# Kernel optimization log

Hardware: AMD Instinct MI355X
Metric: run time of the kernel (lower is better)

The kernel has to match this reference:

```python
import math
import jax, jax.numpy as jnp
import numpy as np

ANCHORS_SETTINGS = (
    dict(layer='p3', stride=32, size=48, scale=[2 ** (1.0 / 3.0), 2 ** (2.0 / 3.0)], aspect_ratio=[0.667, 1, 1.5]),
    dict(layer='p4', stride=64, size=96, scale=[2 ** (1.0 / 3.0), 2 ** (2.0 / 3.0)], aspect_ratio=[0.667, 1, 1.5]),
    dict(layer='p5', stride=128, size=192, scale=[1, 2 ** (1.0 / 3.0), 2 ** (2.0 / 3.0)], aspect_ratio=[0.667, 1, 1.5]),
)


def anchor_configs():
    # 21 static (kernel, stride, padding) configs, in the exact counter order of
    # weighted_anchor_aggregator (p3 x6, p4 x6, p5 x9).
    cfgs = []
    for info in ANCHORS_SETTINGS:
        stride, size = info['stride'], info['size']
        for scale in info['scale']:
            for ar in info['aspect_ratio']:
                kernel = (int(size * scale / float(ar) ** 0.5), int(size * scale * float(ar) ** 0.5))
                padding = (math.ceil((kernel[0] - stride) / 2.0), math.ceil((kernel[1] - stride) / 2.0))
                cfgs.append((kernel, (stride, stride), padding))
    return cfgs


def extract_weighted_patches(x, weights, kernel, stride, padding):
    # x: (B,H,W,C); weights: (B,k,gh,gw). Vectorized equivalent of the original
    # lax.scan over per-position dynamic_slice gathers:
    #   acc = sum_{i,j} weights[:,:,i,j] (x) x_pad[:, i*s : i*s+kh, j*s : j*s+kw, :]
    b = x.shape[0]
    _, k, gh, gw = weights.shape
    xp = jnp.pad(x, ((0, 0),
                     (padding[0], padding[0] + kernel[0]),
                     (padding[1], padding[1] + kernel[1]),
                     (0, 0)))
    rows = jnp.arange(gh)[:, None] * stride[0] + jnp.arange(kernel[0])[None, :]  # (gh, kh)
    cols = jnp.arange(gw)[:, None] * stride[1] + jnp.arange(kernel[1])[None, :]  # (gw, kw)
    # gather all strided patches: (B, gh, kh, gw, kw, C)
    patches = xp[:, rows][:, :, :, cols]
    # weighted sum over grid positions -> (B, k, kh, kw, C)
    return jnp.einsum('bkij,bihjwc->bkhwc', weights, patches)


def _aggregate(x, weights_p3, weights_p4, weights_p5):
    weights = ([weights_p3[:, a] for a in range(weights_p3.shape[1])]
               + [weights_p4[:, a] for a in range(weights_p4.shape[1])]
               + [weights_p5[:, a] for a in range(weights_p5.shape[1])])
    b, k = weights[0].shape[0], weights[0].shape[1]
    acc = jnp.zeros((b * k, 224, 224, 3), x.dtype)
    for w, (kernel, stride, padding) in zip(weights, anchor_configs()):
        agg = extract_weighted_patches(x, w, kernel, stride, padding)
        agg = agg.reshape(b * k, kernel[0], kernel[1], 3)
        acc = acc + jax.image.resize(agg, (b * k, 224, 224, 3), 'bilinear')
    return acc


def setup_inputs() -> dict:
    key = jax.random.key(0)
    k0, k1, k2, k3 = jax.random.split(key, 4)
    B, K = 8, 4
    return {
        'x': jax.random.normal(k0, (B, 448, 448, 3), jnp.float32),
        'weights_p3': jax.random.uniform(k1, (B, 6, K, 14, 14), jnp.float32),
        'weights_p4': jax.random.uniform(k2, (B, 6, K, 7, 7), jnp.float32),
        'weights_p5': jax.random.uniform(k3, (B, 9, K, 4, 4), jnp.float32),
    }


def reference(x, weights_p3, weights_p4, weights_p5):
    return _aggregate(x, weights_p3, weights_p4, weights_p5)
```

## Files before the change

### kernel.cpp

```cpp
#include <hip/hip_runtime.h>
#include <math.h>


#define BATCH 8
#define KK 4
#define OUT_HW 224
#define IMG_HW 448
#define NCFG 21

#define WTBL_BYTES (NCFG * 2 * OUT_HW * 16)
#define ITBL_BYTES (NCFG * 2 * OUT_HW * 4)
#define WT_OFF_BYTES (WTBL_BYTES + ITBL_BYTES)
#define WT_F4 12912
#define AGG_OFF_BYTES (WT_OFF_BYTES + WT_F4 * 16)

#define REGION_PX 640

struct CfgEntry {
    int kh, kw;
    int mth, mtw;
    int tbl;
    int ws_off;
};

struct GroupArgs {
    CfgEntry e[NCFG];
    int n;
};

struct ACfg {
    int kh, kw, p0, p1;
    int layer;
    int qpr;
    int wt_off;
    int ws_off;
    int block_start;
    int blocks_per_img;
};

struct AggArgs {
    ACfg e[NCFG];
    int n;
};

struct TablesArgs { int kh[NCFG]; int kw[NCFG]; };

struct TrArgs {
    int layer[NCFG];
    int anchor[NCFG];
    int gsz[NCFG];
    int wt_off[NCFG];
};

struct F3 { float a, b, c; };
struct F6 { float f[6]; };

__device__ inline unsigned int bf16_rne(float f) {
    unsigned int u = __float_as_uint(f);
    return (u + 0x7fffu + ((u >> 16) & 1u)) >> 16;
}

__global__ __launch_bounds__(256) void init_tables(float4* __restrict__ wtbl,
                                                   int* __restrict__ itbl,
                                                   TablesArgs t) {
    int cfg = blockIdx.x >> 1;
    int dim = blockIdx.x & 1;
    int o = threadIdx.x;
    if (o >= OUT_HW) return;
    int n = dim ? t.kw[cfg] : t.kh[cfg];

    float inv = (float)(1.0 / ((double)OUT_HW / (double)n));
    float ks  = inv > 1.f ? inv : 1.f;
    float rks = 1.f / ks;
    float sf  = ((float)o + 0.5f) * inv - 0.5f;
    int i0 = (int)ceilf(sf - ks);  if (i0 < 0) i0 = 0;
    int i1 = (int)floorf(sf + ks); if (i1 > n - 1) i1 = n - 1;
    float sum = 0.f;
    for (int i = i0; i <= i1; ++i) {
        float v = 1.f - fabsf((float)i - sf) * rks;
        sum += (v > 0.f ? v : 0.f);
    }
    float rsum = 1.f / sum;
    float w[4];
#pragma unroll
    for (int d = 0; d < 4; ++d) {
        int i = i0 + d;
        float v = 0.f;
        if (i <= i1) {
            v = 1.f - fabsf((float)i - sf) * rks;
            v = (v > 0.f ? v : 0.f) * rsum;
        }
        w[d] = v;
    }
    int idx = cfg * (2 * OUT_HW) + dim * OUT_HW + o;
    wtbl[idx] = make_float4(w[0], w[1], w[2], w[3]);
    itbl[idx] = i0;
}

__global__ __launch_bounds__(256) void transpose_w(
        const float* __restrict__ wp3, const float* __restrict__ wp4,
        const float* __restrict__ wp5, float4* __restrict__ wT, TrArgs t) {
    int cfg = blockIdx.x;
    int b = blockIdx.y;
    int gsz = t.gsz[cfg];
    const float* base;
    int A;
    if (t.layer[cfg] == 0)      { base = wp3; A = 6; }
    else if (t.layer[cfg] == 1) { base = wp4; A = 6; }
    else                        { base = wp5; A = 9; }
    const float* src = base + (size_t)(b * A + t.anchor[cfg]) * (KK * gsz);
    for (int g = threadIdx.x; g < gsz; g += 256) {
        wT[t.wt_off[cfg] + b * gsz + g] =
            make_float4(src[0 * gsz + g], src[1 * gsz + g],
                        src[2 * gsz + g], src[3 * gsz + g]);
    }
}

template <int GH, int GW, int STRIDE>
__device__ inline void agg_body(const ACfg& c, int b, int h, int w0,
                                const float* __restrict__ xb,
                                const float4* __restrict__ wlds,
                                uint2* __restrict__ agg) {
    float acc[2][4][3] = {};

    const int rb = h - c.p0;
    int ilo = rb >= 0 ? 0 : (-rb + STRIDE - 1) / STRIDE;
    int ihi = (IMG_HW - 1 - rb) / STRIDE;
    if (ihi > GH - 1) ihi = GH - 1;

    const int cb = w0 - c.p1;

#pragma unroll 1
    for (int i = ilo; i <= ihi; ++i) {
        const float* xr = xb + (size_t)(rb + i * STRIDE) * (IMG_HW * 3);
        const float4* wrow = wlds + i * GW;
#pragma unroll
        for (int j = 0; j < GW; ++j) {
            int col = cb + j * STRIDE;
            float xv[6];
            bool any;
            if ((unsigned)col <= (unsigned)(IMG_HW - 2)) {
                F6 v = *(const F6*)(xr + (size_t)col * 3);
#pragma unroll
                for (int q = 0; q < 6; ++q) xv[q] = v.f[q];
                any = true;
            } else {
                bool ok0 = (unsigned)col < (unsigned)IMG_HW;
                bool ok1 = (unsigned)(col + 1) < (unsigned)IMG_HW;
                any = ok0 || ok1;
#pragma unroll
                for (int q = 0; q < 6; ++q) xv[q] = 0.f;
                if (ok0) {
                    F3 v = *(const F3*)(xr + (size_t)col * 3);
                    xv[0] = v.a; xv[1] = v.b; xv[2] = v.c;
                }
                if (ok1) {
                    F3 v = *(const F3*)(xr + (size_t)(col + 1) * 3);
                    xv[3] = v.a; xv[4] = v.b; xv[5] = v.c;
                }
            }
            if (any) {
                float4 wk = wrow[j];
#pragma unroll
                for (int t = 0; t < 2; ++t) {
                    float x0 = xv[t * 3 + 0], x1 = xv[t * 3 + 1], x2 = xv[t * 3 + 2];
                    acc[t][0][0] = fmaf(wk.x, x0, acc[t][0][0]);
                    acc[t][0][1] = fmaf(wk.x, x1, acc[t][0][1]);
                    acc[t][0][2] = fmaf(wk.x, x2, acc[t][0][2]);
                    acc[t][1][0] = fmaf(wk.y, x0, acc[t][1][0]);
                    acc[t][1][1] = fmaf(wk.y, x1, acc[t][1][1]);
                    acc[t][1][2] = fmaf(wk.y, x2, acc[t][1][2]);
                    acc[t][2][0] = fmaf(wk.z, x0, acc[t][2][0]);
                    acc[t][2][1] = fmaf(wk.z, x1, acc[t][2][1]);
                    acc[t][2][2] = fmaf(wk.z, x2, acc[t][2][2]);
                    acc[t][3][0] = fmaf(wk.w, x0, acc[t][3][0]);
                    acc[t][3][1] = fmaf(wk.w, x1, acc[t][3][1]);
                    acc[t][3][2] = fmaf(wk.w, x2, acc[t][3][2]);
                }
            }
        }
    }

    const int npix = c.kh * c.kw;
    const bool two = (w0 + 1) < c.kw;
#pragma unroll
    for (int k = 0; k < 4; ++k) {
        size_t base = (size_t)c.ws_off + (size_t)(b * KK + k) * npix
                    + (size_t)h * c.kw + w0;
        uint2 o0;
        o0.x = bf16_rne(acc[0][k][0]) | (bf16_rne(acc[0][k][1]) << 16);
        o0.y = bf16_rne(acc[0][k][2]);
        agg[base] = o0;
        if (two) {
            uint2 o1;
            o1.x = bf16_rne(acc[1][k][0]) | (bf16_rne(acc[1][k][1]) << 16);
            o1.y = bf16_rne(acc[1][k][2]);
            agg[base + 1] = o1;
        }
    }
}

__global__ __launch_bounds__(256, 4) void agg_all(
        const float* __restrict__ x,
        const float4* __restrict__ wT,
        uint2* __restrict__ agg,
        AggArgs a) {
    int bid = blockIdx.x;
    int ci = 0;
    while (ci + 1 < a.n && bid >= a.e[ci + 1].block_start) ci++;
    const ACfg c = a.e[ci];
    int local = bid - c.block_start;
    int b     = local / c.blocks_per_img;
    int sblk  = local - b * c.blocks_per_img;

    const int gsz = (c.layer == 0) ? 196 : (c.layer == 1) ? 49 : 16;
    __shared__ float4 wlds[196];
    for (int t = threadIdx.x; t < gsz; t += 256)
        wlds[t] = wT[c.wt_off + b * gsz + t];
    __syncthreads();

    int pidx = sblk * 256 + (int)threadIdx.x;
    if (pidx >= c.kh * c.qpr) return;
    int h  = pidx / c.qpr;
    int w0 = (pidx - h * c.qpr) * 2;

    const float* __restrict__ xb = x + (size_t)b * (IMG_HW * IMG_HW * 3);
    if (c.layer == 0)      agg_body<14, 14, 32>(c, b, h, w0, xb, wlds, agg);
    else if (c.layer == 1) agg_body<7, 7, 64>(c, b, h, w0, xb, wlds, agg);
    else                   agg_body<4, 4, 128>(c, b, h, w0, xb, wlds, agg);
}

template <int TH, int TW>
__device__ inline void taps(const uint2* __restrict__ rp0, int rcols,
                            float4 wh4, float4 ww4,
                            float& a0, float& a1, float& a2) {
    const float* wh = (const float*)&wh4;
    const float* ww = (const float*)&ww4;
#pragma unroll
    for (int d = 0; d < TH; ++d) {
        const uint2* rp = rp0 + d * rcols;
        float r0 = 0.f, r1 = 0.f, r2 = 0.f;
#pragma unroll
        for (int e = 0; e < TW; ++e) {
            uint2 v = rp[e];
            float c0 = __uint_as_float(v.x << 16);
            float c1 = __uint_as_float(v.x & 0xffff0000u);
            float c2 = __uint_as_float(v.y << 16);
            float w = ww[e];
            r0 = fmaf(w, c0, r0);
            r1 = fmaf(w, c1, r1);
            r2 = fmaf(w, c2, r2);
        }
        a0 = fmaf(wh[d], r0, a0);
        a1 = fmaf(wh[d], r1, a1);
        a2 = fmaf(wh[d], r2, a2);
    }
}

struct Win { int ri0, ci0, rrows, rcols; };

__global__ __launch_bounds__(256) void resize_kernel(
        const uint2* __restrict__ agg,
        const float4* __restrict__ wtbl,
        const int* __restrict__ itbl,
        float* __restrict__ out,
        GroupArgs g, int accumulate) {
    const int tid = threadIdx.x;
    const int tx = tid & 15;
    const int ty = tid >> 4;
    const int xo = blockIdx.x * 16 + tx;
    const int yo = blockIdx.y * 16 + ty;
    const int bk0 = blockIdx.z * 2;

    __shared__ float4 wlds[NCFG * 32];
    __shared__ int    ilds[NCFG * 32];
    __shared__ uint2  region[2 * REGION_PX];

    const int nent = g.n * 32;
    for (int e = tid; e < nent; e += 256) {
        int ci  = e >> 5;
        int r   = e & 31;
        int isW = r >> 4;
        int idx = r & 15;
        int base_o = isW ? (blockIdx.x * 16) : (blockIdx.y * 16);
        int src = g.e[ci].tbl * (2 * OUT_HW) + isW * OUT_HW + base_o + idx;
        wlds[ci * 32 + r] = wtbl[src];
        ilds[ci * 32 + r] = itbl[src];
    }
    __syncthreads();

    const int scc = tid & 31;
    const int srw = tid >> 5;

    uint2 sreg[2][4];
    Win wn, wc;

    {
        const CfgEntry c0 = g.e[0];
        int ri0 = ilds[0 * 32 + 0];
        int ri1 = ilds[0 * 32 + 15] + c0.mth - 1;
        int ci0 = ilds[0 * 32 + 16];
        int ci1 = ilds[0 * 32 + 31] + c0.mtw - 1;
        wn.ri0 = ri0; wn.ci0 = ci0;
        wn.rrows = ri1 - ri0 + 1; wn.rcols = ci1 - ci0 + 1;
        const int npx = c0.kh * c0.kw;
        const uint2* base = agg + (size_t)c0.ws_off + (size_t)bk0 * npx;
        int gj = ci0 + scc; if (gj > c0.kw - 1) gj = c0.kw - 1;
        bool cok = scc < wn.rcols;
#pragma unroll
        for (int s = 0; s < 4; ++s) {
            int r = srw + s * 8;
            if (cok && r < wn.rrows) {
                int gi = ri0 + r; if (gi > c0.kh - 1) gi = c0.kh - 1;
                size_t o = (size_t)gi * c0.kw + gj;
                sreg[0][s] = base[o];
                sreg[1][s] = base[o + npx];
            }
        }
    }

    size_t ob0 = (((size_t)bk0 * OUT_HW + yo) * OUT_HW + xo) * 3;
    size_t ob1 = ob0 + (size_t)OUT_HW * OUT_HW * 3;
    float a0, a1, a2, b0, b1, b2;
    if (accumulate) {
        a0 = out[ob0]; a1 = out[ob0 + 1]; a2 = out[ob0 + 2];
        b0 = out[ob1]; b1 = out[ob1 + 1]; b2 = out[ob1 + 2];
    } else {
        a0 = a1 = a2 = b0 = b1 = b2 = 0.f;
    }

    for (int c = 0; c < g.n; ++c) {
        wc = wn;
        __syncthreads();
        {
            bool cok = scc < wc.rcols;
#pragma unroll
            for (int s = 0; s < 4; ++s) {
                int r = srw + s * 8;
                if (cok && r < wc.rrows) {
                    int o = r * wc.rcols + scc;
                    region[o] = sreg[0][s];
                    region[REGION_PX + o] = sreg[1][s];
                }
            }
        }
        __syncthreads();

        if (c + 1 < g.n) {
            const CfgEntry cn = g.e[c + 1];
            int ri0 = ilds[(c + 1) * 32 + 0];
            int ri1 = ilds[(c + 1) * 32 + 15] + cn.mth - 1;
            int ci0 = ilds[(c + 1) * 32 + 16];
            int ci1 = ilds[(c + 1) * 32 + 31] + cn.mtw - 1;
            wn.ri0 = ri0; wn.ci0 = ci0;
            wn.rrows = ri1 - ri0 + 1; wn.rcols = ci1 - ci0 + 1;
            const int npx = cn.kh * cn.kw;
            const uint2* base = agg + (size_t)cn.ws_off + (size_t)bk0 * npx;
            int gj = ci0 + scc; if (gj > cn.kw - 1) gj = cn.kw - 1;
            bool cok = scc < wn.rcols;
#pragma unroll
            for (int s = 0; s < 4; ++s) {
                int r = srw + s * 8;
                if (cok && r < wn.rrows) {
                    int gi = ri0 + r; if (gi > cn.kh - 1) gi = cn.kh - 1;
                    size_t o = (size_t)gi * cn.kw + gj;
                    sreg[0][s] = base[o];
                    sreg[1][s] = base[o + npx];
                }
            }
        }

        float4 wh4 = wlds[c * 32 + ty];
        float4 ww4 = wlds[c * 32 + 16 + tx];
        int i0 = ilds[c * 32 + ty];
        int j0 = ilds[c * 32 + 16 + tx];
        int roff = (i0 - wc.ri0) * wc.rcols + (j0 - wc.ci0);
        const uint2* rp0 = region + roff;
        const uint2* rp1 = region + REGION_PX + roff;

        switch ((g.e[c].mth << 2) | g.e[c].mtw) {
            case (2 << 2) | 2:
                taps<2, 2>(rp0, wc.rcols, wh4, ww4, a0, a1, a2);
                taps<2, 2>(rp1, wc.rcols, wh4, ww4, b0, b1, b2); break;
            case (3 << 2) | 2:
                taps<3, 2>(rp0, wc.rcols, wh4, ww4, a0, a1, a2);
                taps<3, 2>(rp1, wc.rcols, wh4, ww4, b0, b1, b2); break;
            case (2 << 2) | 3:
                taps<2, 3>(rp0, wc.rcols, wh4, ww4, a0, a1, a2);
                taps<2, 3>(rp1, wc.rcols, wh4, ww4, b0, b1, b2); break;
            case (3 << 2) | 3:
                taps<3, 3>(rp0, wc.rcols, wh4, ww4, a0, a1, a2);
                taps<3, 3>(rp1, wc.rcols, wh4, ww4, b0, b1, b2); break;
            case (4 << 2) | 3:
                taps<4, 3>(rp0, wc.rcols, wh4, ww4, a0, a1, a2);
                taps<4, 3>(rp1, wc.rcols, wh4, ww4, b0, b1, b2); break;
            case (3 << 2) | 4:
                taps<3, 4>(rp0, wc.rcols, wh4, ww4, a0, a1, a2);
                taps<3, 4>(rp1, wc.rcols, wh4, ww4, b0, b1, b2); break;
            default:
                taps<4, 4>(rp0, wc.rcols, wh4, ww4, a0, a1, a2);
                taps<4, 4>(rp1, wc.rcols, wh4, ww4, b0, b1, b2); break;
        }
    }

    out[ob0 + 0] = a0; out[ob0 + 1] = a1; out[ob0 + 2] = a2;
    out[ob1 + 0] = b0; out[ob1 + 1] = b1; out[ob1 + 2] = b2;
}

extern "C" void kernel_launch(void* const* d_in, const int* in_sizes, int n_in,
                              void* d_out, int out_size, void* d_ws, size_t ws_size,
                              hipStream_t stream) {
    const float* x   = (const float*)d_in[0];
    const float* wp3 = (const float*)d_in[1];
    const float* wp4 = (const float*)d_in[2];
    const float* wp5 = (const float*)d_in[3];
    float* out = (float*)d_out;
    float4* wtbl = (float4*)d_ws;
    int*    itbl = (int*)((char*)d_ws + WTBL_BYTES);
    float4* wT   = (float4*)((char*)d_ws + WT_OFF_BYTES);
    uint2*  agg  = (uint2*)((char*)d_ws + AGG_OFF_BYTES);

    struct { int stride, size, nscale; double scales[3]; int gh; } layers[3] = {
        {32, 48, 2, {pow(2.0, 1.0 / 3.0), pow(2.0, 2.0 / 3.0), 0.0}, 14},
        {64, 96, 2, {pow(2.0, 1.0 / 3.0), pow(2.0, 2.0 / 3.0), 0.0}, 7},
        {128, 192, 3, {1.0, pow(2.0, 1.0 / 3.0), pow(2.0, 2.0 / 3.0)}, 4},
    };
    const double ars[3] = {0.667, 1.0, 1.5};

    struct HostCfg {
        int kh, kw, stride, p0, p1, gh, gw, layer, anchor, mth, mtw, wt_off;
        int qpr, blocks_per_img;
    } cfg[NCFG];
    TablesArgs ta;
    TrArgs tr;
    int nc = 0, wt_run = 0;
    for (int L = 0; L < 3; ++L) {
        int anchor = 0;
        for (int si = 0; si < layers[L].nscale; ++si) {
            for (int ai = 0; ai < 3; ++ai) {
                double ss = (double)layers[L].size * layers[L].scales[si];
                double sq = pow(ars[ai], 0.5);
                int kh = (int)(ss / sq);
                int kw = (int)(ss * sq);
                HostCfg& e = cfg[nc];
                e.kh = kh; e.kw = kw;
                e.stride = layers[L].stride;
                e.p0 = (int)ceil((double)(kh - layers[L].stride) / 2.0);
                e.p1 = (int)ceil((double)(kw - layers[L].stride) / 2.0);
                e.gh = layers[L].gh; e.gw = layers[L].gh;
                e.layer = L; e.anchor = anchor++;
                e.mth = (kh < OUT_HW) ? 2 : (int)((2.0 * kh) / OUT_HW) + 1;
                e.mtw = (kw < OUT_HW) ? 2 : (int)((2.0 * kw) / OUT_HW) + 1;
                if (e.mth > 4) e.mth = 4;
                if (e.mtw > 4) e.mtw = 4;
                e.qpr = (kw + 1) / 2;
                e.blocks_per_img = (kh * e.qpr + 255) / 256;
                e.wt_off = wt_run;
                int gsz = e.gh * e.gw;
                wt_run += BATCH * gsz;
                ta.kh[nc] = kh; ta.kw[nc] = kw;
                tr.layer[nc] = L; tr.anchor[nc] = e.anchor;
                tr.gsz[nc] = gsz; tr.wt_off[nc] = e.wt_off;
                ++nc;
            }
        }
    }

    init_tables<<<NCFG * 2, 256, 0, stream>>>(wtbl, itbl, ta);
    transpose_w<<<dim3(NCFG, BATCH), 256, 0, stream>>>(wp3, wp4, wp5, wT, tr);

    size_t cap_px = (ws_size - AGG_OFF_BYTES) / 8;
    dim3 rgrid(OUT_HW / 16, OUT_HW / 16, BATCH * KK / 2);

    int i = 0;
    int first = 1;
    while (i < NCFG) {
        int gstart = i;
        size_t used = 0;
        while (i < NCFG) {
            size_t need = (size_t)cfg[i].kh * cfg[i].kw * (BATCH * KK);
            if (i > gstart && used + need > cap_px) break;
            used += need;
            ++i;
            if (used >= cap_px) break;
        }
        GroupArgs g; g.n = 0;
        AggArgs aa; aa.n = 0;
        int ablocks = 0;
        size_t off = 0;
        for (int c = gstart; c < i; ++c) {
            ACfg& lc = aa.e[aa.n++];
            lc.kh = cfg[c].kh; lc.kw = cfg[c].kw;
            lc.p0 = cfg[c].p0; lc.p1 = cfg[c].p1;
            lc.layer = cfg[c].layer;
            lc.qpr = cfg[c].qpr;
            lc.wt_off = cfg[c].wt_off;
            lc.ws_off = (int)off;
            lc.block_start = ablocks;
            lc.blocks_per_img = cfg[c].blocks_per_img;
            ablocks += cfg[c].blocks_per_img * BATCH;
            CfgEntry& re = g.e[g.n++];
            re.kh = cfg[c].kh; re.kw = cfg[c].kw;
            re.mth = cfg[c].mth; re.mtw = cfg[c].mtw;
            re.tbl = c; re.ws_off = (int)off;
            off += (size_t)cfg[c].kh * cfg[c].kw * (BATCH * KK);
        }
        agg_all<<<ablocks, 256, 0, stream>>>(x, wT, agg, aa);
        resize_kernel<<<rgrid, 256, 0, stream>>>(agg, wtbl, itbl, out, g, first ? 0 : 1);
        first = 0;
    }
    (void)in_sizes; (void)n_in; (void)out_size;
}
```

Measured before the change: 330.6 us.

## Split bilinear resize into separable row and column passes

Replaces the fused 2D resize kernel, which staged agg windows in shared memory and evaluated all taps per output pixel, with two separable passes. A row pass writes a bf16 intermediate of shape 224 x kw per config, and a column pass accumulates every config into the output. The agg kernel's block index is also reordered so the batch comes from the low bits. The change lowers per-output tap arithmetic but adds an extra global round trip through the intermediate and rounds it to bf16 a second time. It also uses more workspace, which may force more groups and therefore more launches.

Result: slower. 457.5 us (+38.4%).

```diff
diff --git a/kernel.cpp b/kernel.cpp
--- a/kernel.cpp
+++ b/kernel.cpp
@@ -12,21 +12,7 @@
 #define ITBL_BYTES (NCFG * 2 * OUT_HW * 4)
 #define WT_OFF_BYTES (WTBL_BYTES + ITBL_BYTES)
 #define WT_F4 12912
-#define AGG_OFF_BYTES (WT_OFF_BYTES + WT_F4 * 16)
-
-#define REGION_PX 640
-
-struct CfgEntry {
-    int kh, kw;
-    int mth, mtw;
-    int tbl;
-    int ws_off;
-};
-
-struct GroupArgs {
-    CfgEntry e[NCFG];
-    int n;
-};
+#define POOL_OFF_BYTES (WT_OFF_BYTES + WT_F4 * 16)
 
 struct ACfg {
     int kh, kw, p0, p1;
@@ -40,6 +26,21 @@
 
 struct AggArgs {
     ACfg e[NCFG];
+    int n;
+};
+
+struct RCfg {
+    int kh, kw;
+    int mth, mtw;
+    int tbl;
+    int agg_off;
+    int tmp_off;
+    int b1_start;
+    unsigned kwmagic;
+};
+
+struct RArgs {
+    RCfg e[NCFG];
     int n;
 };
 
@@ -205,13 +206,12 @@
         const float4* __restrict__ wT,
         uint2* __restrict__ agg,
         AggArgs a) {
-    int bid = blockIdx.x;
+    int b = blockIdx.x & 7;
+    int q = blockIdx.x >> 3;
     int ci = 0;
-    while (ci + 1 < a.n && bid >= a.e[ci + 1].block_start) ci++;
+    while (ci + 1 < a.n && q >= a.e[ci + 1].block_start) ci++;
     const ACfg c = a.e[ci];
-    int local = bid - c.block_start;
-    int b     = local / c.blocks_per_img;
-    int sblk  = local - b * c.blocks_per_img;
+    int sblk = q - c.block_start;
 
     const int gsz = (c.layer == 0) ? 196 : (c.layer == 1) ? 49 : 16;
     __shared__ float4 wlds[196];
@@ -230,181 +230,92 @@
     else                   agg_body<4, 4, 128>(c, b, h, w0, xb, wlds, agg);
 }
 
-template <int TH, int TW>
-__device__ inline void taps(const uint2* __restrict__ rp0, int rcols,
-                            float4 wh4, float4 ww4,
-                            float& a0, float& a1, float& a2) {
-    const float* wh = (const float*)&wh4;
-    const float* ww = (const float*)&ww4;
-#pragma unroll
-    for (int d = 0; d < TH; ++d) {
-        const uint2* rp = rp0 + d * rcols;
-        float r0 = 0.f, r1 = 0.f, r2 = 0.f;
-#pragma unroll
-        for (int e = 0; e < TW; ++e) {
-            uint2 v = rp[e];
-            float c0 = __uint_as_float(v.x << 16);
-            float c1 = __uint_as_float(v.x & 0xffff0000u);
-            float c2 = __uint_as_float(v.y << 16);
-            float w = ww[e];
-            r0 = fmaf(w, c0, r0);
-            r1 = fmaf(w, c1, r1);
-            r2 = fmaf(w, c2, r2);
-        }
-        a0 = fmaf(wh[d], r0, a0);
-        a1 = fmaf(wh[d], r1, a1);
-        a2 = fmaf(wh[d], r2, a2);
-    }
-}
-
-struct Win { int ri0, ci0, rrows, rcols; };
-
-__global__ __launch_bounds__(256) void resize_kernel(
+__global__ __launch_bounds__(256) void row_resize(
         const uint2* __restrict__ agg,
+        uint2* __restrict__ tmp,
+        const float4* __restrict__ wtbl,
+        const int* __restrict__ itbl,
+        RArgs ra) {
+    int bid = blockIdx.x;
+    int ci = 0;
+    while (ci + 1 < ra.n && bid >= ra.e[ci + 1].b1_start) ci++;
+    const RCfg c = ra.e[ci];
+    int idx = (bid - c.b1_start) * 256 + (int)threadIdx.x;
+    if (idx >= BATCH * KK * OUT_HW * c.kw) return;
+
+    unsigned uq = __umulhi((unsigned)idx, c.kwmagic);
+    int w = idx - (int)uq * c.kw;
+    if (w < 0) { uq--; w += c.kw; }
+    else if (w >= c.kw) { uq++; w -= c.kw; }
+    int y  = (int)(uq % OUT_HW);
+    int bk = (int)(uq / OUT_HW);
+
+    int ti = c.tbl * (2 * OUT_HW) + y;
+    float4 wh = wtbl[ti];
+    int i0 = itbl[ti];
+    const float* whp = (const float*)&wh;
+
+    const uint2* ab = agg + (size_t)c.agg_off + (size_t)bk * c.kh * c.kw + w;
+    float a0 = 0.f, a1 = 0.f, a2 = 0.f;
+    const int taps = c.mth;
+#pragma unroll
+    for (int d = 0; d < 4; ++d) {
+        if (d < taps) {
+            int r = i0 + d; if (r > c.kh - 1) r = c.kh - 1;
+            uint2 v = ab[(size_t)r * c.kw];
+            float wd = whp[d];
+            a0 = fmaf(wd, __uint_as_float(v.x << 16), a0);
+            a1 = fmaf(wd, __uint_as_float(v.x & 0xffff0000u), a1);
+            a2 = fmaf(wd, __uint_as_float(v.y << 16), a2);
+        }
+    }
+    uint2 o;
+    o.x = bf16_rne(a0) | (bf16_rne(a1) << 16);
+    o.y = bf16_rne(a2);
+    tmp[(size_t)c.tmp_off + idx] = o;
+}
+
+__global__ __launch_bounds__(256) void col_resize(
+        const uint2* __restrict__ tmp,
         const float4* __restrict__ wtbl,
         const int* __restrict__ itbl,
         float* __restrict__ out,
-        GroupArgs g, int accumulate) {
-    const int tid = threadIdx.x;
-    const int tx = tid & 15;
-    const int ty = tid >> 4;
-    const int xo = blockIdx.x * 16 + tx;
-    const int yo = blockIdx.y * 16 + ty;
-    const int bk0 = blockIdx.z * 2;
-
-    __shared__ float4 wlds[NCFG * 32];
-    __shared__ int    ilds[NCFG * 32];
-    __shared__ uint2  region[2 * REGION_PX];
-
-    const int nent = g.n * 32;
-    for (int e = tid; e < nent; e += 256) {
-        int ci  = e >> 5;
-        int r   = e & 31;
-        int isW = r >> 4;
-        int idx = r & 15;
-        int base_o = isW ? (blockIdx.x * 16) : (blockIdx.y * 16);
-        int src = g.e[ci].tbl * (2 * OUT_HW) + isW * OUT_HW + base_o + idx;
-        wlds[ci * 32 + r] = wtbl[src];
-        ilds[ci * 32 + r] = itbl[src];
-    }
-    __syncthreads();
-
-    const int scc = tid & 31;
-    const int srw = tid >> 5;
-
-    uint2 sreg[2][4];
-    Win wn, wc;
-
-    {
-        const CfgEntry c0 = g.e[0];
-        int ri0 = ilds[0 * 32 + 0];
-        int ri1 = ilds[0 * 32 + 15] + c0.mth - 1;
-        int ci0 = ilds[0 * 32 + 16];
-        int ci1 = ilds[0 * 32 + 31] + c0.mtw - 1;
-        wn.ri0 = ri0; wn.ci0 = ci0;
-        wn.rrows = ri1 - ri0 + 1; wn.rcols = ci1 - ci0 + 1;
-        const int npx = c0.kh * c0.kw;
-        const uint2* base = agg + (size_t)c0.ws_off + (size_t)bk0 * npx;
-        int gj = ci0 + scc; if (gj > c0.kw - 1) gj = c0.kw - 1;
-        bool cok = scc < wn.rcols;
-#pragma unroll
-        for (int s = 0; s < 4; ++s) {
-            int r = srw + s * 8;
-            if (cok && r < wn.rrows) {
-                int gi = ri0 + r; if (gi > c0.kh - 1) gi = c0.kh - 1;
-                size_t o = (size_t)gi * c0.kw + gj;
-                sreg[0][s] = base[o];
-                sreg[1][s] = base[o + npx];
+        RArgs ra, int accumulate) {
+    int x = threadIdx.x;
+    if (x >= OUT_HW) return;
+    int y  = blockIdx.x;
+    int bk = blockIdx.y;
+
+    size_t ob = (((size_t)bk * OUT_HW + y) * OUT_HW + x) * 3;
+    float a0, a1, a2;
+    if (accumulate) { a0 = out[ob]; a1 = out[ob + 1]; a2 = out[ob + 2]; }
+    else            { a0 = 0.f; a1 = 0.f; a2 = 0.f; }
+
+    for (int ci = 0; ci < ra.n; ++ci) {
+        const int kw = ra.e[ci].kw;
+        int ti = ra.e[ci].tbl * (2 * OUT_HW) + OUT_HW + x;
+        float4 ww = wtbl[ti];
+        int j0 = itbl[ti];
+        const float* wwp = (const float*)&ww;
+        const uint2* tb = tmp + (size_t)ra.e[ci].tmp_off
+                              + ((size_t)bk * OUT_HW + y) * kw;
+        const int taps = ra.e[ci].mtw;
+#pragma unroll
+        for (int e = 0; e < 4; ++e) {
+            if (e < taps) {
+                int col = j0 + e; if (col > kw - 1) col = kw - 1;
+                uint2 v = tb[col];
+                float we = wwp[e];
+                a0 = fmaf(we, __uint_as_float(v.x << 16), a0);
+                a1 = fmaf(we, __uint_as_float(v.x & 0xffff0000u), a1);
+                a2 = fmaf(we, __uint_as_float(v.y << 16), a2);
             }
         }
     }
 
-    size_t ob0 = (((size_t)bk0 * OUT_HW + yo) * OUT_HW + xo) * 3;
-    size_t ob1 = ob0 + (size_t)OUT_HW * OUT_HW * 3;
-    float a0, a1, a2, b0, b1, b2;
-    if (accumulate) {
-        a0 = out[ob0]; a1 = out[ob0 + 1]; a2 = out[ob0 + 2];
-        b0 = out[ob1]; b1 = out[ob1 + 1]; b2 = out[ob1 + 2];
-    } else {
-        a0 = a1 = a2 = b0 = b1 = b2 = 0.f;
-    }
-
-    for (int c = 0; c < g.n; ++c) {
-        wc = wn;
-        __syncthreads();
-        {
-            bool cok = scc < wc.rcols;
-#pragma unroll
-            for (int s = 0; s < 4; ++s) {
-                int r = srw + s * 8;
-                if (cok && r < wc.rrows) {
-                    int o = r * wc.rcols + scc;
-                    region[o] = sreg[0][s];
-                    region[REGION_PX + o] = sreg[1][s];
-                }
-            }
-        }
-        __syncthreads();
-
-        if (c + 1 < g.n) {
-            const CfgEntry cn = g.e[c + 1];
-            int ri0 = ilds[(c + 1) * 32 + 0];
-            int ri1 = ilds[(c + 1) * 32 + 15] + cn.mth - 1;
-            int ci0 = ilds[(c + 1) * 32 + 16];
-            int ci1 = ilds[(c + 1) * 32 + 31] + cn.mtw - 1;
-            wn.ri0 = ri0; wn.ci0 = ci0;
-            wn.rrows = ri1 - ri0 + 1; wn.rcols = ci1 - ci0 + 1;
-            const int npx = cn.kh * cn.kw;
-            const uint2* base = agg + (size_t)cn.ws_off + (size_t)bk0 * npx;
-            int gj = ci0 + scc; if (gj > cn.kw - 1) gj = cn.kw - 1;
-            bool cok = scc < wn.rcols;
-#pragma unroll
-            for (int s = 0; s < 4; ++s) {
-                int r = srw + s * 8;
-                if (cok && r < wn.rrows) {
-                    int gi = ri0 + r; if (gi > cn.kh - 1) gi = cn.kh - 1;
-                    size_t o = (size_t)gi * cn.kw + gj;
-                    sreg[0][s] = base[o];
-                    sreg[1][s] = base[o + npx];
-                }
-            }
-        }
-
-        float4 wh4 = wlds[c * 32 + ty];
-        float4 ww4 = wlds[c * 32 + 16 + tx];
-        int i0 = ilds[c * 32 + ty];
-        int j0 = ilds[c * 32 + 16 + tx];
-        int roff = (i0 - wc.ri0) * wc.rcols + (j0 - wc.ci0);
-        const uint2* rp0 = region + roff;
-        const uint2* rp1 = region + REGION_PX + roff;
-
-        switch ((g.e[c].mth << 2) | g.e[c].mtw) {
-            case (2 << 2) | 2:
-                taps<2, 2>(rp0, wc.rcols, wh4, ww4, a0, a1, a2);
-                taps<2, 2>(rp1, wc.rcols, wh4, ww4, b0, b1, b2); break;
-            case (3 << 2) | 2:
-                taps<3, 2>(rp0, wc.rcols, wh4, ww4, a0, a1, a2);
-                taps<3, 2>(rp1, wc.rcols, wh4, ww4, b0, b1, b2); break;
-            case (2 << 2) | 3:
-                taps<2, 3>(rp0, wc.rcols, wh4, ww4, a0, a1, a2);
-                taps<2, 3>(rp1, wc.rcols, wh4, ww4, b0, b1, b2); break;
-            case (3 << 2) | 3:
-                taps<3, 3>(rp0, wc.rcols, wh4, ww4, a0, a1, a2);
-                taps<3, 3>(rp1, wc.rcols, wh4, ww4, b0, b1, b2); break;
-            case (4 << 2) | 3:
-                taps<4, 3>(rp0, wc.rcols, wh4, ww4, a0, a1, a2);
-                taps<4, 3>(rp1, wc.rcols, wh4, ww4, b0, b1, b2); break;
-            case (3 << 2) | 4:
-                taps<3, 4>(rp0, wc.rcols, wh4, ww4, a0, a1, a2);
-                taps<3, 4>(rp1, wc.rcols, wh4, ww4, b0, b1, b2); break;
-            default:
-                taps<4, 4>(rp0, wc.rcols, wh4, ww4, a0, a1, a2);
-                taps<4, 4>(rp1, wc.rcols, wh4, ww4, b0, b1, b2); break;
-        }
-    }
-
-    out[ob0 + 0] = a0; out[ob0 + 1] = a1; out[ob0 + 2] = a2;
-    out[ob1 + 0] = b0; out[ob1 + 1] = b1; out[ob1 + 2] = b2;
+    out[ob + 0] = a0;
+    out[ob + 1] = a1;
+    out[ob + 2] = a2;
 }
 
 extern "C" void kernel_launch(void* const* d_in, const int* in_sizes, int n_in,
@@ -418,7 +329,7 @@
     float4* wtbl = (float4*)d_ws;
     int*    itbl = (int*)((char*)d_ws + WTBL_BYTES);
     float4* wT   = (float4*)((char*)d_ws + WT_OFF_BYTES);
-    uint2*  agg  = (uint2*)((char*)d_ws + AGG_OFF_BYTES);
+    uint2*  pool = (uint2*)((char*)d_ws + POOL_OFF_BYTES);
 
     struct { int stride, size, nscale; double scales[3]; int gh; } layers[3] = {
         {32, 48, 2, {pow(2.0, 1.0 / 3.0), pow(2.0, 2.0 / 3.0), 0.0}, 14},
@@ -469,8 +380,8 @@
     init_tables<<<NCFG * 2, 256, 0, stream>>>(wtbl, itbl, ta);
     transpose_w<<<dim3(NCFG, BATCH), 256, 0, stream>>>(wp3, wp4, wp5, wT, tr);
 
-    size_t cap_px = (ws_size - AGG_OFF_BYTES) / 8;
-    dim3 rgrid(OUT_HW / 16, OUT_HW / 16, BATCH * KK / 2);
+    size_t cap_px = (ws_size - POOL_OFF_BYTES) / 8;
+    dim3 cgrid(OUT_HW, BATCH * KK);
 
     int i = 0;
     int first = 1;
@@ -478,15 +389,17 @@
         int gstart = i;
         size_t used = 0;
         while (i < NCFG) {
-            size_t need = (size_t)cfg[i].kh * cfg[i].kw * (BATCH * KK);
+            size_t need = ((size_t)cfg[i].kh * cfg[i].kw
+                         + (size_t)OUT_HW * cfg[i].kw) * (BATCH * KK);
             if (i > gstart && used + need > cap_px) break;
             used += need;
             ++i;
             if (used >= cap_px) break;
         }
-        GroupArgs g; g.n = 0;
         AggArgs aa; aa.n = 0;
-        int ablocks = 0;
+        RArgs ra; ra.n = 0;
+        int T = 0;
+        int b1_blocks = 0;
         size_t off = 0;
         for (int c = gstart; c < i; ++c) {
             ACfg& lc = aa.e[aa.n++];
@@ -496,17 +409,27 @@
             lc.qpr = cfg[c].qpr;
             lc.wt_off = cfg[c].wt_off;
             lc.ws_off = (int)off;
-            lc.block_start = ablocks;
+            lc.block_start = T;
             lc.blocks_per_img = cfg[c].blocks_per_img;
-            ablocks += cfg[c].blocks_per_img * BATCH;
-            CfgEntry& re = g.e[g.n++];
-            re.kh = cfg[c].kh; re.kw = cfg[c].kw;
-            re.mth = cfg[c].mth; re.mtw = cfg[c].mtw;
-            re.tbl = c; re.ws_off = (int)off;
+            T += cfg[c].blocks_per_img;
+
+            RCfg& rc = ra.e[ra.n++];
+            rc.kh = cfg[c].kh; rc.kw = cfg[c].kw;
+            rc.mth = cfg[c].mth; rc.mtw = cfg[c].mtw;
+            rc.tbl = c;
+            rc.agg_off = (int)off;
             off += (size_t)cfg[c].kh * cfg[c].kw * (BATCH * KK);
-        }
-        agg_all<<<ablocks, 256, 0, stream>>>(x, wT, agg, aa);
-        resize_kernel<<<rgrid, 256, 0, stream>>>(agg, wtbl, itbl, out, g, first ? 0 : 1);
+            rc.tmp_off = (int)off;
+            off += (size_t)OUT_HW * cfg[c].kw * (BATCH * KK);
+            rc.b1_start = b1_blocks;
+            b1_blocks += (BATCH * KK * OUT_HW * cfg[c].kw + 255) / 256;
+            rc.kwmagic = (unsigned)((0x100000000ULL + cfg[c].kw - 1)
+                                    / (unsigned long long)cfg[c].kw);
+        }
+        agg_all<<<8 * T, 256, 0, stream>>>(x, wT, pool, aa);
+        row_resize<<<b1_blocks, 256, 0, stream>>>(pool, pool, wtbl, itbl, ra);
+        col_resize<<<cgrid, 256, 0, stream>>>(pool, wtbl, itbl, out, ra,
+                                              first ? 0 : 1);
         first = 0;
     }
     (void)in_sizes; (void)n_in; (void)out_size;
```

## Restructure agg block order, unroll coarse layers, one image per resize block

Applied to the files above, without the earlier changes.

The aggregation kernel now interleaves batch images in the block index (batch = blockIdx & 7), so neighbouring blocks share a config and weight table. The p4/p5 layers get a fully unrolled row loop with per-row bounds checks instead of a runtime loop. The resize kernel now handles one (b,k) image per block instead of two, and decodes bf16 into a float4 shared region once per load rather than in every tap. This doubles the resize grid and the shared-memory footprint per pixel, and cuts per-block register pressure and the bf16 unpack work inside the inner loop.

After: 332.5 us. About the same (+0.6%).

```diff
diff --git a/kernel.cpp b/kernel.cpp
--- a/kernel.cpp
+++ b/kernel.cpp
@@ -12,7 +12,7 @@
 #define ITBL_BYTES (NCFG * 2 * OUT_HW * 4)
 #define WT_OFF_BYTES (WTBL_BYTES + ITBL_BYTES)
 #define WT_F4 12912
-#define AGG_OFF_BYTES (WT_OFF_BYTES + WT_F4 * 16)
+#define POOL_OFF_BYTES (WT_OFF_BYTES + WT_F4 * 16)
 
 #define REGION_PX 640
 
@@ -116,7 +116,51 @@
     }
 }
 
-template <int GH, int GW, int STRIDE>
+__device__ inline void agg_tap(const float* __restrict__ xr, int col,
+                               float4 wk, float acc[2][4][3]) {
+    float xv[6];
+    bool any;
+    if ((unsigned)col <= (unsigned)(IMG_HW - 2)) {
+        F6 v = *(const F6*)(xr + (size_t)col * 3);
+#pragma unroll
+        for (int q = 0; q < 6; ++q) xv[q] = v.f[q];
+        any = true;
+    } else {
+        bool ok0 = (unsigned)col < (unsigned)IMG_HW;
+        bool ok1 = (unsigned)(col + 1) < (unsigned)IMG_HW;
+        any = ok0 || ok1;
+#pragma unroll
+        for (int q = 0; q < 6; ++q) xv[q] = 0.f;
+        if (ok0) {
+            F3 v = *(const F3*)(xr + (size_t)col * 3);
+            xv[0] = v.a; xv[1] = v.b; xv[2] = v.c;
+        }
+        if (ok1) {
+            F3 v = *(const F3*)(xr + (size_t)(col + 1) * 3);
+            xv[3] = v.a; xv[4] = v.b; xv[5] = v.c;
+        }
+    }
+    if (any) {
+#pragma unroll
+        for (int t = 0; t < 2; ++t) {
+            float x0 = xv[t * 3 + 0], x1 = xv[t * 3 + 1], x2 = xv[t * 3 + 2];
+            acc[t][0][0] = fmaf(wk.x, x0, acc[t][0][0]);
+            acc[t][0][1] = fmaf(wk.x, x1, acc[t][0][1]);
+            acc[t][0][2] = fmaf(wk.x, x2, acc[t][0][2]);
+            acc[t][1][0] = fmaf(wk.y, x0, acc[t][1][0]);
+            acc[t][1][1] = fmaf(wk.y, x1, acc[t][1][1]);
+            acc[t][1][2] = fmaf(wk.y, x2, acc[t][1][2]);
+            acc[t][2][0] = fmaf(wk.z, x0, acc[t][2][0]);
+            acc[t][2][1] = fmaf(wk.z, x1, acc[t][2][1]);
+            acc[t][2][2] = fmaf(wk.z, x2, acc[t][2][2]);
+            acc[t][3][0] = fmaf(wk.w, x0, acc[t][3][0]);
+            acc[t][3][1] = fmaf(wk.w, x1, acc[t][3][1]);
+            acc[t][3][2] = fmaf(wk.w, x2, acc[t][3][2]);
+        }
+    }
+}
+
+template <int GH, int GW, int STRIDE, bool FULL>
 __device__ inline void agg_body(const ACfg& c, int b, int h, int w0,
                                 const float* __restrict__ xb,
                                 const float4* __restrict__ wlds,
@@ -124,60 +168,30 @@
     float acc[2][4][3] = {};
 
     const int rb = h - c.p0;
-    int ilo = rb >= 0 ? 0 : (-rb + STRIDE - 1) / STRIDE;
-    int ihi = (IMG_HW - 1 - rb) / STRIDE;
-    if (ihi > GH - 1) ihi = GH - 1;
-
     const int cb = w0 - c.p1;
 
+    if constexpr (FULL) {
+#pragma unroll
+        for (int i = 0; i < GH; ++i) {
+            int row = rb + i * STRIDE;
+            if ((unsigned)row < (unsigned)IMG_HW) {
+                const float* xr = xb + (size_t)row * (IMG_HW * 3);
+#pragma unroll
+                for (int j = 0; j < GW; ++j)
+                    agg_tap(xr, cb + j * STRIDE, wlds[i * GW + j], acc);
+            }
+        }
+    } else {
+        int ilo = rb >= 0 ? 0 : (-rb + STRIDE - 1) / STRIDE;
+        int ihi = (IMG_HW - 1 - rb) / STRIDE;
+        if (ihi > GH - 1) ihi = GH - 1;
 #pragma unroll 1
-    for (int i = ilo; i <= ihi; ++i) {
-        const float* xr = xb + (size_t)(rb + i * STRIDE) * (IMG_HW * 3);
-        const float4* wrow = wlds + i * GW;
-#pragma unroll
-        for (int j = 0; j < GW; ++j) {
-            int col = cb + j * STRIDE;
-            float xv[6];
-            bool any;
-            if ((unsigned)col <= (unsigned)(IMG_HW - 2)) {
-                F6 v = *(const F6*)(xr + (size_t)col * 3);
-#pragma unroll
-                for (int q = 0; q < 6; ++q) xv[q] = v.f[q];
-                any = true;
-            } else {
-                bool ok0 = (unsigned)col < (unsigned)IMG_HW;
-                bool ok1 = (unsigned)(col + 1) < (unsigned)IMG_HW;
-                any = ok0 || ok1;
-#pragma unroll
-                for (int q = 0; q < 6; ++q) xv[q] = 0.f;
-                if (ok0) {
-                    F3 v = *(const F3*)(xr + (size_t)col * 3);
-                    xv[0] = v.a; xv[1] = v.b; xv[2] = v.c;
-                }
-                if (ok1) {
-                    F3 v = *(const F3*)(xr + (size_t)(col + 1) * 3);
-                    xv[3] = v.a; xv[4] = v.b; xv[5] = v.c;
-                }
-            }
-            if (any) {
-                float4 wk = wrow[j];
-#pragma unroll
-                for (int t = 0; t < 2; ++t) {
-                    float x0 = xv[t * 3 + 0], x1 = xv[t * 3 + 1], x2 = xv[t * 3 + 2];
-                    acc[t][0][0] = fmaf(wk.x, x0, acc[t][0][0]);
-                    acc[t][0][1] = fmaf(wk.x, x1, acc[t][0][1]);
-                    acc[t][0][2] = fmaf(wk.x, x2, acc[t][0][2]);
-                    acc[t][1][0] = fmaf(wk.y, x0, acc[t][1][0]);
-                    acc[t][1][1] = fmaf(wk.y, x1, acc[t][1][1]);
-                    acc[t][1][2] = fmaf(wk.y, x2, acc[t][1][2]);
-                    acc[t][2][0] = fmaf(wk.z, x0, acc[t][2][0]);
-                    acc[t][2][1] = fmaf(wk.z, x1, acc[t][2][1]);
-                    acc[t][2][2] = fmaf(wk.z, x2, acc[t][2][2]);
-                    acc[t][3][0] = fmaf(wk.w, x0, acc[t][3][0]);
-                    acc[t][3][1] = fmaf(wk.w, x1, acc[t][3][1]);
-                    acc[t][3][2] = fmaf(wk.w, x2, acc[t][3][2]);
-                }
-            }
+        for (int i = ilo; i <= ihi; ++i) {
+            const float* xr = xb + (size_t)(rb + i * STRIDE) * (IMG_HW * 3);
+            const float4* wrow = wlds + i * GW;
+#pragma unroll
+            for (int j = 0; j < GW; ++j)
+                agg_tap(xr, cb + j * STRIDE, wrow[j], acc);
         }
     }
 
@@ -205,13 +219,12 @@
         const float4* __restrict__ wT,
         uint2* __restrict__ agg,
         AggArgs a) {
-    int bid = blockIdx.x;
+    int b = blockIdx.x & 7;
+    int q = blockIdx.x >> 3;
     int ci = 0;
-    while (ci + 1 < a.n && bid >= a.e[ci + 1].block_start) ci++;
+    while (ci + 1 < a.n && q >= a.e[ci + 1].block_start) ci++;
     const ACfg c = a.e[ci];
-    int local = bid - c.block_start;
-    int b     = local / c.blocks_per_img;
-    int sblk  = local - b * c.blocks_per_img;
+    int sblk = q - c.block_start;
 
     const int gsz = (c.layer == 0) ? 196 : (c.layer == 1) ? 49 : 16;
     __shared__ float4 wlds[196];
@@ -225,31 +238,28 @@
     int w0 = (pidx - h * c.qpr) * 2;
 
     const float* __restrict__ xb = x + (size_t)b * (IMG_HW * IMG_HW * 3);
-    if (c.layer == 0)      agg_body<14, 14, 32>(c, b, h, w0, xb, wlds, agg);
-    else if (c.layer == 1) agg_body<7, 7, 64>(c, b, h, w0, xb, wlds, agg);
-    else                   agg_body<4, 4, 128>(c, b, h, w0, xb, wlds, agg);
+    if (c.layer == 0)      agg_body<14, 14, 32, false>(c, b, h, w0, xb, wlds, agg);
+    else if (c.layer == 1) agg_body<7, 7, 64, true>(c, b, h, w0, xb, wlds, agg);
+    else                   agg_body<4, 4, 128, true>(c, b, h, w0, xb, wlds, agg);
 }
 
 template <int TH, int TW>
-__device__ inline void taps(const uint2* __restrict__ rp0, int rcols,
+__device__ inline void taps(const float4* __restrict__ rp0, int rcols,
                             float4 wh4, float4 ww4,
                             float& a0, float& a1, float& a2) {
     const float* wh = (const float*)&wh4;
     const float* ww = (const float*)&ww4;
 #pragma unroll
     for (int d = 0; d < TH; ++d) {
-        const uint2* rp = rp0 + d * rcols;
+        const float4* rp = rp0 + d * rcols;
         float r0 = 0.f, r1 = 0.f, r2 = 0.f;
 #pragma unroll
         for (int e = 0; e < TW; ++e) {
-            uint2 v = rp[e];
-            float c0 = __uint_as_float(v.x << 16);
-            float c1 = __uint_as_float(v.x & 0xffff0000u);
-            float c2 = __uint_as_float(v.y << 16);
+            float4 v = rp[e];
             float w = ww[e];
-            r0 = fmaf(w, c0, r0);
-            r1 = fmaf(w, c1, r1);
-            r2 = fmaf(w, c2, r2);
+            r0 = fmaf(w, v.x, r0);
+            r1 = fmaf(w, v.y, r1);
+            r2 = fmaf(w, v.z, r2);
         }
         a0 = fmaf(wh[d], r0, a0);
         a1 = fmaf(wh[d], r1, a1);
@@ -270,11 +280,11 @@
     const int ty = tid >> 4;
     const int xo = blockIdx.x * 16 + tx;
     const int yo = blockIdx.y * 16 + ty;
-    const int bk0 = blockIdx.z * 2;
+    const int bk = blockIdx.z;
 
     __shared__ float4 wlds[NCFG * 32];
     __shared__ int    ilds[NCFG * 32];
-    __shared__ uint2  region[2 * REGION_PX];
+    __shared__ float4 region[REGION_PX];
 
     const int nent = g.n * 32;
     for (int e = tid; e < nent; e += 256) {
@@ -292,7 +302,7 @@
     const int scc = tid & 31;
     const int srw = tid >> 5;
 
-    uint2 sreg[2][4];
+    uint2 sreg[4];
     Win wn, wc;
 
     {
@@ -303,8 +313,7 @@
         int ci1 = ilds[0 * 32 + 31] + c0.mtw - 1;
         wn.ri0 = ri0; wn.ci0 = ci0;
         wn.rrows = ri1 - ri0 + 1; wn.rcols = ci1 - ci0 + 1;
-        const int npx = c0.kh * c0.kw;
-        const uint2* base = agg + (size_t)c0.ws_off + (size_t)bk0 * npx;
+        const uint2* base = agg + (size_t)c0.ws_off + (size_t)bk * c0.kh * c0.kw;
         int gj = ci0 + scc; if (gj > c0.kw - 1) gj = c0.kw - 1;
         bool cok = scc < wn.rcols;
 #pragma unroll
@@ -312,22 +321,15 @@
             int r = srw + s * 8;
             if (cok && r < wn.rrows) {
                 int gi = ri0 + r; if (gi > c0.kh - 1) gi = c0.kh - 1;
-                size_t o = (size_t)gi * c0.kw + gj;
-                sreg[0][s] = base[o];
-                sreg[1][s] = base[o + npx];
+                sreg[s] = base[(size_t)gi * c0.kw + gj];
             }
         }
     }
 
-    size_t ob0 = (((size_t)bk0 * OUT_HW + yo) * OUT_HW + xo) * 3;
-    size_t ob1 = ob0 + (size_t)OUT_HW * OUT_HW * 3;
-    float a0, a1, a2, b0, b1, b2;
-    if (accumulate) {
-        a0 = out[ob0]; a1 = out[ob0 + 1]; a2 = out[ob0 + 2];
-        b0 = out[ob1]; b1 = out[ob1 + 1]; b2 = out[ob1 + 2];
-    } else {
-        a0 = a1 = a2 = b0 = b1 = b2 = 0.f;
-    }
+    size_t obase = (((size_t)bk * OUT_HW + yo) * OUT_HW + xo) * 3;
+    float a0, a1, a2;
+    if (accumulate) { a0 = out[obase]; a1 = out[obase + 1]; a2 = out[obase + 2]; }
+    else            { a0 = 0.f; a1 = 0.f; a2 = 0.f; }
 
     for (int c = 0; c < g.n; ++c) {
         wc = wn;
@@ -338,9 +340,11 @@
             for (int s = 0; s < 4; ++s) {
                 int r = srw + s * 8;
                 if (cok && r < wc.rrows) {
-                    int o = r * wc.rcols + scc;
-                    region[o] = sreg[0][s];
-                    region[REGION_PX + o] = sreg[1][s];
+                    uint2 v = sreg[s];
+                    region[r * wc.rcols + scc] = make_float4(
+                        __uint_as_float(v.x << 16),
+                        __uint_as_float(v.x & 0xffff0000u),
+                        __uint_as_float(v.y << 16), 0.f);
                 }
             }
         }
@@ -354,8 +358,7 @@
             int ci1 = ilds[(c + 1) * 32 + 31] + cn.mtw - 1;
             wn.ri0 = ri0; wn.ci0 = ci0;
             wn.rrows = ri1 - ri0 + 1; wn.rcols = ci1 - ci0 + 1;
-            const int npx = cn.kh * cn.kw;
-            const uint2* base = agg + (size_t)cn.ws_off + (size_t)bk0 * npx;
+            const uint2* base = agg + (size_t)cn.ws_off + (size_t)bk * cn.kh * cn.kw;
             int gj = ci0 + scc; if (gj > cn.kw - 1) gj = cn.kw - 1;
             bool cok = scc < wn.rcols;
 #pragma unroll
@@ -363,9 +366,7 @@
                 int r = srw + s * 8;
                 if (cok && r < wn.rrows) {
                     int gi = ri0 + r; if (gi > cn.kh - 1) gi = cn.kh - 1;
-                    size_t o = (size_t)gi * cn.kw + gj;
-                    sreg[0][s] = base[o];
-                    sreg[1][s] = base[o + npx];
+                    sreg[s] = base[(size_t)gi * cn.kw + gj];
                 }
             }
         }
@@ -374,37 +375,22 @@
         float4 ww4 = wlds[c * 32 + 16 + tx];
         int i0 = ilds[c * 32 + ty];
         int j0 = ilds[c * 32 + 16 + tx];
-        int roff = (i0 - wc.ri0) * wc.rcols + (j0 - wc.ci0);
-        const uint2* rp0 = region + roff;
-        const uint2* rp1 = region + REGION_PX + roff;
+        const float4* rp0 = region + (i0 - wc.ri0) * wc.rcols + (j0 - wc.ci0);
 
         switch ((g.e[c].mth << 2) | g.e[c].mtw) {
-            case (2 << 2) | 2:
-                taps<2, 2>(rp0, wc.rcols, wh4, ww4, a0, a1, a2);
-                taps<2, 2>(rp1, wc.rcols, wh4, ww4, b0, b1, b2); break;
-            case (3 << 2) | 2:
-                taps<3, 2>(rp0, wc.rcols, wh4, ww4, a0, a1, a2);
-                taps<3, 2>(rp1, wc.rcols, wh4, ww4, b0, b1, b2); break;
-            case (2 << 2) | 3:
-                taps<2, 3>(rp0, wc.rcols, wh4, ww4, a0, a1, a2);
-                taps<2, 3>(rp1, wc.rcols, wh4, ww4, b0, b1, b2); break;
-            case (3 << 2) | 3:
-                taps<3, 3>(rp0, wc.rcols, wh4, ww4, a0, a1, a2);
-                taps<3, 3>(rp1, wc.rcols, wh4, ww4, b0, b1, b2); break;
-            case (4 << 2) | 3:
-                taps<4, 3>(rp0, wc.rcols, wh4, ww4, a0, a1, a2);
-                taps<4, 3>(rp1, wc.rcols, wh4, ww4, b0, b1, b2); break;
-            case (3 << 2) | 4:
-                taps<3, 4>(rp0, wc.rcols, wh4, ww4, a0, a1, a2);
-                taps<3, 4>(rp1, wc.rcols, wh4, ww4, b0, b1, b2); break;
-            default:
-                taps<4, 4>(rp0, wc.rcols, wh4, ww4, a0, a1, a2);
-                taps<4, 4>(rp1, wc.rcols, wh4, ww4, b0, b1, b2); break;
-        }
-    }
-
-    out[ob0 + 0] = a0; out[ob0 + 1] = a1; out[ob0 + 2] = a2;
-    out[ob1 + 0] = b0; out[ob1 + 1] = b1; out[ob1 + 2] = b2;
+            case (2 << 2) | 2: taps<2, 2>(rp0, wc.rcols, wh4, ww4, a0, a1, a2); break;
+            case (3 << 2) | 2: taps<3, 2>(rp0, wc.rcols, wh4, ww4, a0, a1, a2); break;
+            case (2 << 2) | 3: taps<2, 3>(rp0, wc.rcols, wh4, ww4, a0, a1, a2); break;
+            case (3 << 2) | 3: taps<3, 3>(rp0, wc.rcols, wh4, ww4, a0, a1, a2); break;
+            case (4 << 2) | 3: taps<4, 3>(rp0, wc.rcols, wh4, ww4, a0, a1, a2); break;
+            case (3 << 2) | 4: taps<3, 4>(rp0, wc.rcols, wh4, ww4, a0, a1, a2); break;
+            default:           taps<4, 4>(rp0, wc.rcols, wh4, ww4, a0, a1, a2); break;
+        }
+    }
+
+    out[obase + 0] = a0;
+    out[obase + 1] = a1;
+    out[obase + 2] = a2;
 }
 
 extern "C" void kernel_launch(void* const* d_in, const int* in_sizes, int n_in,
@@ -418,7 +404,7 @@
     float4* wtbl = (float4*)d_ws;
     int*    itbl = (int*)((char*)d_ws + WTBL_BYTES);
     float4* wT   = (float4*)((char*)d_ws + WT_OFF_BYTES);
-    uint2*  agg  = (uint2*)((char*)d_ws + AGG_OFF_BYTES);
+    uint2*  pool = (uint2*)((char*)d_ws + POOL_OFF_BYTES);
 
     struct { int stride, size, nscale; double scales[3]; int gh; } layers[3] = {
         {32, 48, 2, {pow(2.0, 1.0 / 3.0), pow(2.0, 2.0 / 3.0), 0.0}, 14},
@@ -469,8 +455,8 @@
     init_tables<<<NCFG * 2, 256, 0, stream>>>(wtbl, itbl, ta);
     transpose_w<<<dim3(NCFG, BATCH), 256, 0, stream>>>(wp3, wp4, wp5, wT, tr);
 
-    size_t cap_px = (ws_size - AGG_OFF_BYTES) / 8;
-    dim3 rgrid(OUT_HW / 16, OUT_HW / 16, BATCH * KK / 2);
+    size_t cap_px = (ws_size - POOL_OFF_BYTES) / 8;
+    dim3 rgrid(OUT_HW / 16, OUT_HW / 16, BATCH * KK);
 
     int i = 0;
     int first = 1;
@@ -484,9 +470,9 @@
             ++i;
             if (used >= cap_px) break;
         }
+        AggArgs aa; aa.n = 0;
         GroupArgs g; g.n = 0;
-        AggArgs aa; aa.n = 0;
-        int ablocks = 0;
+        int T = 0;
         size_t off = 0;
         for (int c = gstart; c < i; ++c) {
             ACfg& lc = aa.e[aa.n++];
@@ -496,17 +482,19 @@
             lc.qpr = cfg[c].qpr;
             lc.wt_off = cfg[c].wt_off;
             lc.ws_off = (int)off;
-            lc.block_start = ablocks;
+            lc.block_start = T;
             lc.blocks_per_img = cfg[c].blocks_per_img;
-            ablocks += cfg[c].blocks_per_img * BATCH;
+            T += cfg[c].blocks_per_img;
+
             CfgEntry& re = g.e[g.n++];
             re.kh = cfg[c].kh; re.kw = cfg[c].kw;
             re.mth = cfg[c].mth; re.mtw = cfg[c].mtw;
             re.tbl = c; re.ws_off = (int)off;
             off += (size_t)cfg[c].kh * cfg[c].kw * (BATCH * KK);
         }
-        agg_all<<<ablocks, 256, 0, stream>>>(x, wT, agg, aa);
-        resize_kernel<<<rgrid, 256, 0, stream>>>(agg, wtbl, itbl, out, g, first ? 0 : 1);
+        agg_all<<<8 * T, 256, 0, stream>>>(x, wT, pool, aa);
+        resize_kernel<<<rgrid, 256, 0, stream>>>(pool, wtbl, itbl, out, g,
+                                                 first ? 0 : 1);
         first = 0;
     }
     (void)in_sizes; (void)n_in; (void)out_size;
```
